# Kernel optimization log

Measured on AMD Instinct MI355X. Metric: run time of the kernel, lower is better.

Reference implementation:

```python
import jax, jax.numpy as jnp
import numpy as np

D_MODEL = 1024
D_FF = 4096
N_EXPERTS = 8
D_EXPERT = D_FF // N_EXPERTS  # 512
TOP_K = 2
LB_WEIGHT = 0.01
B, S = 4, 2048


def setup_inputs() -> dict:
    key = jax.random.key(0)
    ks = jax.random.split(key, 8)
    x = jax.random.normal(ks[0], (B, S, D_MODEL), dtype=jnp.float32)
    # per-expert FFN params stacked on expert axis
    w1 = jax.random.normal(ks[1], (N_EXPERTS, D_MODEL, D_EXPERT), dtype=jnp.float32) * (1.0 / np.sqrt(D_MODEL))
    b1 = jnp.zeros((N_EXPERTS, D_EXPERT), dtype=jnp.float32)
    w2 = jax.random.normal(ks[2], (N_EXPERTS, D_EXPERT, D_MODEL), dtype=jnp.float32) * (1.0 / np.sqrt(D_EXPERT))
    b2 = jnp.zeros((N_EXPERTS, D_MODEL), dtype=jnp.float32)
    centroids = jax.random.normal(ks[3], (N_EXPERTS, D_MODEL), dtype=jnp.float32) * 0.02
    w_route = jax.random.normal(ks[4], (N_EXPERTS, D_MODEL), dtype=jnp.float32) * (1.0 / np.sqrt(D_MODEL))
    return {"x": x, "w1": w1, "b1": b1, "w2": w2, "b2": b2,
            "centroids": centroids, "w_route": w_route}


def _top_k_softmax(logits, k):
    # softmax restricted to the top-k logits per token; zeros elsewhere
    vals, _ = jax.lax.top_k(logits, k)          # (..., k)
    thresh = vals[..., -1:]                     # kth-largest value
    masked = jnp.where(logits >= thresh, logits, -jnp.inf)
    return jax.nn.softmax(masked, axis=-1)


def reference(x, w1, b1, w2, b2, centroids, w_route):
    eps = 1e-12
    x_norm = x / jnp.maximum(jnp.linalg.norm(x, axis=-1, keepdims=True), eps)
    c_norm = centroids / jnp.maximum(jnp.linalg.norm(centroids, axis=-1, keepdims=True), eps)
    cos_scores = jnp.einsum('bsd,ed->bse', x_norm, c_norm)
    route_scores = jnp.einsum('bsd,ed->bse', x, w_route)
    logits = cos_scores + route_scores                       # (B,S,E)
    gates = _top_k_softmax(logits, TOP_K)                    # (B,S,E)
    # all experts computed on all tokens (dense MoE, masked combine)
    h = jax.nn.gelu(jnp.einsum('bsd,edh->bseh', x, w1) + b1, approximate=False)
    expert_out = jnp.einsum('bseh,ehd->bsed', h, w2) + b2    # (B,S,E,D)
    out = jnp.einsum('bse,bsed->bsd', gates, expert_out)
    return out
```

## Files before the change

kernel.cpp:

```cpp
#include <hip/hip_runtime.h>
#include <hip/hip_bf16.h>
#include <math.h>

#define T_TOK 8192
#define DM 1024
#define DE 512
#define NE 8
#define DFF 4096

#define CO_X   0
#define CO_W1  8388608
#define CO_W2  12582912
#define CO_B1  16777216
#define CO_B2  16781312
#define CO_CE  16789504
#define CO_WR  16797696
#define CO_TOT 16805888

#define WS_GATE2 256
#define WS_B32   65792
#define WS_TOP2  262400
#define WS_TOK   295168
#define WS_AE    360704
#define WS_AG    426240
#define WS_INV   491776
#define WS_CONV  557312
#define WS_HC    34169088
#define WS_OC    50946304

typedef __attribute__((ext_vector_type(8))) __bf16 bf16x8;
typedef __attribute__((ext_vector_type(4))) __bf16 bf16x4;
typedef __attribute__((ext_vector_type(4))) float f32x4;

__device__ __forceinline__ f32x4 ld4(const void* p, size_t off, int md)
{
  f32x4 r;
  if (md){
    bf16x4 v = *(const bf16x4*)((const __bf16*)p + off);
    #pragma unroll
    for (int j = 0; j < 4; j++) r[j] = (float)v[j];
  } else {
    r = *(const f32x4*)((const float*)p + off);
  }
  return r;
}

__device__ __forceinline__ void async_ld16(const __bf16* g, __bf16* l)
{
  __builtin_amdgcn_global_load_lds(
      (const __attribute__((address_space(1))) unsigned int*)g,
      (__attribute__((address_space(3))) unsigned int*)l, 16, 0, 0);
}

__global__ __launch_bounds__(256) void detect_k(const void* xp, const void* cp,
                                                int* meta, int* b32)
{
  const int tid = threadIdx.x;
  const float* xf = (const float*)xp;
  int ok = 0;
  for (int i = tid; i < 1024; i += 256){
    float a = fabsf(xf[i]);
    if (a > 1e-8f && a < 100.f) ok++;
  }
  __shared__ int cnt;
  __shared__ int flg;
  if (tid == 0) cnt = 0;
  __syncthreads();
  atomicAdd(&cnt, ok);
  __syncthreads();
  if (tid == 0){ flg = (cnt > 512) ? 0 : 1; meta[0] = flg; }
  __syncthreads();
  const int md = flg;

  const int e = tid >> 5, i = tid & 31;
  float ss = 0.f;
  for (int j = 0; j < 32; j++){
    size_t d = (size_t)e * DM + i + j * 32;
    float v = md ? (float)((const __bf16*)cp)[d] : ((const float*)cp)[d];
    ss += v * v;
  }
  #pragma unroll
  for (int m = 1; m < 32; m <<= 1) ss += __shfl_xor(ss, m, 64);
  float* cinv = (float*)(meta + 48);
  if (i == 0) cinv[e] = 1.f / fmaxf(sqrtf(ss), 1e-12f);

  b32[tid] = 0;
  if (tid < 8) meta[16 + tid] = 0;
}

__global__ __launch_bounds__(256) void convert_k(
    const float* __restrict__ b1, const float* __restrict__ b2,
    const float* __restrict__ ce, const float* __restrict__ wr,
    __bf16* __restrict__ dst, const int* __restrict__ meta)
{
  if (meta[0]) return;
  const size_t j = ((size_t)blockIdx.x * 256 + threadIdx.x) * 4;
  const float* src;
  const size_t doff = CO_B1 + j;
  if      (j < 4096)  src = b1 + j;
  else if (j < 12288) src = b2 + (j - 4096);
  else if (j < 20480) src = ce + (j - 12288);
  else                src = wr + (j - 20480);
  f32x4 v = *(const f32x4*)src;
  bf16x4 o;
  #pragma unroll
  for (int t = 0; t < 4; t++) o[t] = (__bf16)v[t];
  *(bf16x4*)(dst + doff) = o;
}

__global__ __launch_bounds__(256) void transp_k(
    const void* w1q, const void* w2q, __bf16* __restrict__ conv,
    const int* __restrict__ meta)
{
  const int md = meta[0];
  __shared__ __bf16 tile[32][33];
  const int b = blockIdx.x, tid = threadIdx.x;
  const int ty = tid >> 5, tx = tid & 31;

  const void* src; __bf16* dst; int ldS, ldD, i0, j0; size_t soff, doffb;
  if (b < 4096){
    const int e = b >> 9, t = b & 511;
    i0 = (t >> 4) << 5; j0 = (t & 15) << 5;
    ldS = DE; ldD = DM;
    soff = (size_t)e * DM * DE;
    dst = conv + CO_W1; doffb = (size_t)e * DE * DM;
    src = md ? (const void*)((const __bf16*)w1q) : (const void*)((const float*)w1q);
  } else {
    const int e = (b - 4096) >> 9, t = (b - 4096) & 511;
    i0 = (t >> 5) << 5; j0 = (t & 31) << 5;
    ldS = DM; ldD = DE;
    soff = (size_t)e * DE * DM;
    dst = conv + CO_W2; doffb = (size_t)e * DM * DE;
    src = md ? (const void*)((const __bf16*)w2q) : (const void*)((const float*)w2q);
  }

  #pragma unroll
  for (int rr = 0; rr < 4; rr++){
    const int r = rr * 8 + ty;
    const size_t s = soff + (size_t)(i0 + r) * ldS + j0 + tx;
    tile[r][tx] = md ? ((const __bf16*)src)[s] : (__bf16)((const float*)src)[s];
  }
  __syncthreads();
  #pragma unroll
  for (int rr = 0; rr < 4; rr++){
    const int r = rr * 8 + ty;
    dst[doffb + (size_t)(j0 + r) * ldD + i0 + tx] = tile[tx][r];
  }
}

__global__ __launch_bounds__(256) void route_k(
    const void* __restrict__ xp, const void* __restrict__ cp,
    const void* __restrict__ wp, const int* __restrict__ meta,
    __bf16* __restrict__ conv, float2* __restrict__ gate2,
    int* __restrict__ top2, int* __restrict__ b32)
{
  const int md = meta[0];
  const float* cinv = (const float*)(meta + 48);
  const int tid = threadIdx.x;
  const int g = tid >> 4, l = tid & 15;
  const int t = blockIdx.x * 16 + g;

  __shared__ int hist[8];
  if (tid < 8) hist[tid] = 0;
  __syncthreads();

  float xx = 0.f, cd[NE], wd[NE];
  #pragma unroll
  for (int e = 0; e < NE; e++){ cd[e] = 0.f; wd[e] = 0.f; }

  const size_t xbase = (size_t)t * DM;
  for (int j = 0; j < 16; j++){
    const int d0 = j * 64 + l * 4;
    f32x4 xv = ld4(xp, xbase + d0, md);
    if (!md){
      bf16x4 o;
      #pragma unroll
      for (int jj = 0; jj < 4; jj++) o[jj] = (__bf16)xv[jj];
      *(bf16x4*)(conv + CO_X + xbase + d0) = o;
    }
    xx += xv[0]*xv[0] + xv[1]*xv[1] + xv[2]*xv[2] + xv[3]*xv[3];
    #pragma unroll
    for (int e = 0; e < NE; e++){
      f32x4 cv = ld4(cp, (size_t)e * DM + d0, md);
      f32x4 wv = ld4(wp, (size_t)e * DM + d0, md);
      cd[e] += xv[0]*cv[0] + xv[1]*cv[1] + xv[2]*cv[2] + xv[3]*cv[3];
      wd[e] += xv[0]*wv[0] + xv[1]*wv[1] + xv[2]*wv[2] + xv[3]*wv[3];
    }
  }
  #pragma unroll
  for (int m = 1; m < 16; m <<= 1){
    xx += __shfl_xor(xx, m, 64);
    #pragma unroll
    for (int e = 0; e < NE; e++){
      cd[e] += __shfl_xor(cd[e], m, 64);
      wd[e] += __shfl_xor(wd[e], m, 64);
    }
  }

  if (l == 0){
    const float rxn = 1.f / fmaxf(sqrtf(xx), 1e-12f);
    float logits[NE];
    #pragma unroll
    for (int e = 0; e < NE; e++) logits[e] = cd[e] * rxn * cinv[e] + wd[e];
    float m1 = -1e30f; int i1 = 0;
    #pragma unroll
    for (int e = 0; e < NE; e++) if (logits[e] > m1){ m1 = logits[e]; i1 = e; }
    float m2 = -1e30f; int i2 = (i1 == 0) ? 1 : 0;
    #pragma unroll
    for (int e = 0; e < NE; e++)
      if (e != i1 && logits[e] > m2){ m2 = logits[e]; i2 = e; }
    float denom = 0.f, ex1 = 0.f, ex2 = 0.f;
    #pragma unroll
    for (int e = 0; e < NE; e++){
      if (logits[e] >= m2){
        float ee = expf(logits[e] - m1);
        denom += ee;
        if (e == i1) ex1 = ee;
        if (e == i2) ex2 = ee;
      }
    }
    const float inv = 1.f / denom;
    gate2[t] = make_float2(ex1 * inv, ex2 * inv);
    top2[t] = i1 | (i2 << 8);
    atomicAdd(&hist[i1], 1);
    atomicAdd(&hist[i2], 1);
  }
  __syncthreads();
  if (tid < 8) atomicAdd(&b32[(blockIdx.x >> 4) * 8 + tid], hist[tid]);
}

__global__ void offsets_k(int* meta, int* b32)
{
  const int l = threadIdx.x;
  int running = 0;
  for (int e = 0; e < NE; e++){
    int v = (l < 32) ? b32[l * 8 + e] : 0;
    int incl = v;
    #pragma unroll
    for (int ofs = 1; ofs < 32; ofs <<= 1){
      int n = __shfl_up(incl, ofs, 64);
      if (l >= ofs) incl += n;
    }
    int tot = __shfl(incl, 31, 64);
    if (l < 32) b32[l * 8 + e] = running + (incl - v);
    if (l == 0){ meta[16 + e] = tot; meta[32 + e] = running; }
    running += tot;
  }
}

__global__ __launch_bounds__(256) void place_k(
    const int* __restrict__ top2, const float2* __restrict__ gate2,
    const int* __restrict__ b32, int* __restrict__ tok, int* __restrict__ ae,
    float* __restrict__ agv, int* __restrict__ inv)
{
  __shared__ int cur[8];
  if (threadIdx.x < 8) cur[threadIdx.x] = b32[blockIdx.x * 8 + threadIdx.x];
  __syncthreads();
  const int t = blockIdx.x * 256 + threadIdx.x;
  const int p = top2[t];
  const float2 gg = gate2[t];
  const int e1 = p & 255, e2 = (p >> 8) & 255;
  const int s1 = atomicAdd(&cur[e1], 1);
  tok[s1] = t; ae[s1] = e1; agv[s1] = gg.x; inv[2 * t] = s1;
  const int s2 = atomicAdd(&cur[e2], 1);
  tok[s2] = t; ae[s2] = e2; agv[s2] = gg.y; inv[2 * t + 1] = s2;
}

__device__ __forceinline__ bool find_tile(const int* meta, int tm,
                                          int& e, int& base, int& valid)
{
  for (e = 0; e < NE; e++){
    const int cnt = meta[16 + e];
    const int nt = (cnt + 127) >> 7;
    if (tm < nt){
      const int r0 = tm << 7;
      base = meta[32 + e] + r0;
      valid = cnt - r0;
      return true;
    }
    tm -= nt;
  }
  return false;
}

__device__ __forceinline__ bool find_tile256(const int* meta, int tm,
                                             int& e, int& base, int& valid)
{
  for (e = 0; e < NE; e++){
    const int cnt = meta[16 + e];
    const int nt = (cnt + 255) >> 8;
    if (tm < nt){
      const int r0 = tm << 8;
      base = meta[32 + e] + r0;
      valid = cnt - r0;
      return true;
    }
    tm -= nt;
  }
  return false;
}

__global__ __launch_bounds__(512, 2) void gemm1g_k(
    const void* xq, const void* b1q, const __bf16* __restrict__ conv,
    const int* __restrict__ meta, const int* __restrict__ tok,
    const float* __restrict__ agv, __bf16* __restrict__ Hc)
{
  const int md = meta[0];
  const __bf16* X  = md ? (const __bf16*)xq : conv + CO_X;
  const __bf16* WT = conv + CO_W1;
  const __bf16* bb = md ? (const __bf16*)b1q : conv + CO_B1;

  int e, base, valid;
  if (!find_tile(meta, blockIdx.x, e, base, valid)) return;
  const int n0 = blockIdx.y * 128;

  __shared__ __attribute__((aligned(16))) __bf16 As[2][128 * 64];
  __shared__ __attribute__((aligned(16))) __bf16 Bs[2][128 * 64];

  const int tid = threadIdx.x;
  const int wv = tid >> 6, lane = tid & 63;
  const int q = lane >> 4, ln = lane & 15;
  const int wm = (wv >> 2) * 64, wn = (wv & 3) * 32;
  const int swz = ln & 7;
  f32x4 acc[4][2] = {};

  const int srow = tid >> 3, sch = tid & 7;
  const int sx = ((sch ^ (srow & 7)) << 3);
  const int ta = tok[base + ((srow      < valid) ? srow      : 0)];
  const int tb = tok[base + ((srow + 64 < valid) ? srow + 64 : 0)];
  const __bf16* Ag0 = X + (size_t)ta * DM + sx;
  const __bf16* Ag1 = X + (size_t)tb * DM + sx;
  const __bf16* Bg0 = WT + (size_t)e * (DE * DM) + (size_t)(n0 + srow) * DM + sx;
  const __bf16* Bg1 = Bg0 + (size_t)64 * DM;

  #define G1_STAGE(BUF, K0)                                   \
    do {                                                      \
      async_ld16(Ag0 + (K0), &As[BUF][tid * 8]);              \
      async_ld16(Ag1 + (K0), &As[BUF][tid * 8 + 4096]);       \
      async_ld16(Bg0 + (K0), &Bs[BUF][tid * 8]);              \
      async_ld16(Bg1 + (K0), &Bs[BUF][tid * 8 + 4096]);       \
    } while (0)

  #define G1_COMPUTE(BUF)                                                      \
    do {                                                                       \
      _Pragma("unroll")                                                        \
      for (int kk = 0; kk < 2; kk++){                                          \
        bf16x8 af[4], bfr[2];                                                  \
        const int ch = (((kk << 2) | q) ^ swz) << 3;                           \
        _Pragma("unroll")                                                      \
        for (int mi = 0; mi < 4; mi++)                                         \
          af[mi] = *(const bf16x8*)&As[BUF][(wm + mi * 16 + ln) * 64 + ch];    \
        _Pragma("unroll")                                                      \
        for (int ni = 0; ni < 2; ni++)                                         \
          bfr[ni] = *(const bf16x8*)&Bs[BUF][(wn + ni * 16 + ln) * 64 + ch];   \
        _Pragma("unroll")                                                      \
        for (int mi = 0; mi < 4; mi++)                                         \
          _Pragma("unroll")                                                    \
          for (int ni = 0; ni < 2; ni++)                                       \
            acc[mi][ni] = __builtin_amdgcn_mfma_f32_16x16x32_bf16(             \
                af[mi], bfr[ni], acc[mi][ni], 0, 0, 0);                        \
      }                                                                        \
    } while (0)

  G1_STAGE(0, 0);
  __syncthreads();
  int cr = 0;
  for (int t = 0; t < 16; ++t){
    if (t < 15) G1_STAGE(cr ^ 1, (t + 1) * 64);
    G1_COMPUTE(cr);
    __syncthreads();
    cr ^= 1;
  }
  #undef G1_STAGE
  #undef G1_COMPUTE

  const int coln = n0 + wn;
  float bset[2];
  #pragma unroll
  for (int ni = 0; ni < 2; ni++)
    bset[ni] = (float)bb[e * DE + coln + ni * 16 + ln];
  #pragma unroll
  for (int mi = 0; mi < 4; mi++){
    #pragma unroll
    for (int r = 0; r < 4; r++){
      const int row = wm + mi * 16 + q * 4 + r;
      if (row < valid){
        const int slot = base + row;
        const float g = agv[slot];
        #pragma unroll
        for (int ni = 0; ni < 2; ni++){
          float v = acc[mi][ni][r] + bset[ni];
          float h = 0.5f * v * (1.0f + erff(v * 0.70710678118654752f));
          Hc[(size_t)slot * DE + coln + ni * 16 + ln] = (__bf16)(g * h);
        }
      }
    }
  }
}

__global__ __launch_bounds__(512, 2) void gemm2g_k(
    const __bf16* __restrict__ Hc, const __bf16* __restrict__ conv,
    const int* __restrict__ meta, __bf16* __restrict__ Oc)
{
  const __bf16* WT = conv + CO_W2;

  int e, base, valid;
  if (!find_tile256(meta, blockIdx.x, e, base, valid)) return;
  const int n0 = blockIdx.y * 256;

  __shared__ __attribute__((aligned(16))) __bf16 As[2][256 * 64];
  __shared__ __attribute__((aligned(16))) __bf16 Bs[2][256 * 64];

  const int tid = threadIdx.x;
  const int wv = tid >> 6, lane = tid & 63;
  const int q = lane >> 4, ln = lane & 15;
  const int wm = (wv >> 2) * 128, wn = (wv & 3) * 64;
  const int swz = ln & 7;
  f32x4 acc[8][4] = {};

  const int srow = tid >> 3, sch = tid & 7;
  const int sx = ((sch ^ (srow & 7)) << 3);
  const int r0 = (srow       < valid) ? srow       : 0;
  const int r1 = (srow +  64 < valid) ? srow +  64 : 0;
  const int r2 = (srow + 128 < valid) ? srow + 128 : 0;
  const int r3 = (srow + 192 < valid) ? srow + 192 : 0;
  const __bf16* Ag0 = Hc + (size_t)(base + r0) * DE + sx;
  const __bf16* Ag1 = Hc + (size_t)(base + r1) * DE + sx;
  const __bf16* Ag2 = Hc + (size_t)(base + r2) * DE + sx;
  const __bf16* Ag3 = Hc + (size_t)(base + r3) * DE + sx;
  const __bf16* Bg0 = WT + (size_t)e * (DM * DE) + (size_t)(n0 + srow) * DE + sx;

  #define G2_STAGE(BUF, K0)                                          \
    do {                                                             \
      async_ld16(Ag0 + (K0), &As[BUF][tid * 8]);                     \
      async_ld16(Ag1 + (K0), &As[BUF][tid * 8 + 4096]);              \
      async_ld16(Ag2 + (K0), &As[BUF][tid * 8 + 8192]);              \
      async_ld16(Ag3 + (K0), &As[BUF][tid * 8 + 12288]);             \
      async_ld16(Bg0 + (K0),                &Bs[BUF][tid * 8]);      \
      async_ld16(Bg0 + (K0) +  64 * DE,     &Bs[BUF][tid * 8 + 4096]);  \
      async_ld16(Bg0 + (K0) + 128 * DE,     &Bs[BUF][tid * 8 + 8192]);  \
      async_ld16(Bg0 + (K0) + 192 * DE,     &Bs[BUF][tid * 8 + 12288]); \
    } while (0)

  #define G2_COMPUTE(BUF)                                                      \
    do {                                                                       \
      _Pragma("unroll")                                                        \
      for (int kk = 0; kk < 2; kk++){                                          \
        bf16x8 af[8], bfr[4];                                                  \
        const int ch = (((kk << 2) | q) ^ swz) << 3;                           \
        _Pragma("unroll")                                                      \
        for (int mi = 0; mi < 8; mi++)                                         \
          af[mi] = *(const bf16x8*)&As[BUF][(wm + mi * 16 + ln) * 64 + ch];    \
        _Pragma("unroll")                                                      \
        for (int ni = 0; ni < 4; ni++)                                         \
          bfr[ni] = *(const bf16x8*)&Bs[BUF][(wn + ni * 16 + ln) * 64 + ch];   \
        _Pragma("unroll")                                                      \
        for (int mi = 0; mi < 8; mi++)                                         \
          _Pragma("unroll")                                                    \
          for (int ni = 0; ni < 4; ni++)                                       \
            acc[mi][ni] = __builtin_amdgcn_mfma_f32_16x16x32_bf16(             \
                af[mi], bfr[ni], acc[mi][ni], 0, 0, 0);                        \
      }                                                                        \
    } while (0)

  G2_STAGE(0, 0);
  __syncthreads();
  int cr = 0;
  for (int t = 0; t < 8; ++t){
    if (t < 7) G2_STAGE(cr ^ 1, (t + 1) * 64);
    G2_COMPUTE(cr);
    __syncthreads();
    cr ^= 1;
  }
  #undef G2_STAGE
  #undef G2_COMPUTE

  #pragma unroll
  for (int mi = 0; mi < 8; mi++){
    #pragma unroll
    for (int r = 0; r < 4; r++){
      const int row = wm + mi * 16 + q * 4 + r;
      if (row < valid){
        const int slot = base + row;
        #pragma unroll
        for (int ni = 0; ni < 4; ni++)
          Oc[(size_t)slot * DM + n0 + wn + ni * 16 + ln] = (__bf16)acc[mi][ni][r];
      }
    }
  }
}

__global__ __launch_bounds__(256) void combine_k(
    const __bf16* __restrict__ Oc, const int* __restrict__ inv,
    const int* __restrict__ ae, const float* __restrict__ agv,
    const void* b2q, const int* __restrict__ meta, void* out)
{
  const int md = meta[0];
  const int t = blockIdx.x;
  const int s1 = inv[2 * t], s2 = inv[2 * t + 1];
  const int e1 = ae[s1], e2 = ae[s2];
  const float g1 = agv[s1], g2 = agv[s2];
  const int c = threadIdx.x * 4;

  bf16x4 o1 = *(const bf16x4*)(Oc + (size_t)s1 * DM + c);
  bf16x4 o2 = *(const bf16x4*)(Oc + (size_t)s2 * DM + c);
  f32x4 bv1 = ld4(b2q, (size_t)e1 * DM + c, md);
  f32x4 bv2 = ld4(b2q, (size_t)e2 * DM + c, md);
  f32x4 rr;
  #pragma unroll
  for (int j = 0; j < 4; j++)
    rr[j] = (float)o1[j] + (float)o2[j] + g1 * bv1[j] + g2 * bv2[j];

  if (md){
    bf16x4 ob;
    #pragma unroll
    for (int j = 0; j < 4; j++) ob[j] = (__bf16)rr[j];
    *(bf16x4*)((__bf16*)out + (size_t)t * DM + c) = ob;
  } else {
    *(f32x4*)((float*)out + (size_t)t * DM + c) = rr;
  }
}

extern "C" void kernel_launch(void* const* d_in, const int* in_sizes, int n_in,
                              void* d_out, int out_size, void* d_ws, size_t ws_size,
                              hipStream_t stream)
{
  char* ws = (char*)d_ws;
  int*    meta  = (int*)ws;
  float2* gate2 = (float2*)(ws + WS_GATE2);
  int*    b32   = (int*)(ws + WS_B32);
  int*    top2  = (int*)(ws + WS_TOP2);
  int*    tok   = (int*)(ws + WS_TOK);
  int*    ae    = (int*)(ws + WS_AE);
  float*  agv   = (float*)(ws + WS_AG);
  int*    inv   = (int*)(ws + WS_INV);
  __bf16* conv  = (__bf16*)(ws + WS_CONV);
  __bf16* Hc    = (__bf16*)(ws + WS_HC);
  __bf16* Oc    = (__bf16*)(ws + WS_OC);

  detect_k<<<1, 256, 0, stream>>>(d_in[0], d_in[5], meta, b32);
  transp_k<<<8192, 256, 0, stream>>>(d_in[1], d_in[3], conv, meta);
  convert_k<<<28, 256, 0, stream>>>(
      (const float*)d_in[2], (const float*)d_in[4], (const float*)d_in[5],
      (const float*)d_in[6], conv, meta);
  route_k<<<T_TOK / 16, 256, 0, stream>>>(d_in[0], d_in[5], d_in[6], meta,
                                          conv, gate2, top2, b32);
  offsets_k<<<1, 64, 0, stream>>>(meta, b32);
  place_k<<<T_TOK / 256, 256, 0, stream>>>(top2, gate2, b32, tok, ae, agv, inv);
  gemm1g_k<<<dim3(136, 4), 512, 0, stream>>>(d_in[0], d_in[2], conv, meta,
                                             tok, agv, Hc);
  gemm2g_k<<<dim3(72, 4), 512, 0, stream>>>(Hc, conv, meta, Oc);
  combine_k<<<T_TOK, 256, 0, stream>>>(Oc, inv, ae, agv, d_in[4], meta, d_out);
}
```

Before: 250.5 us.

## Use 256x256 tiles in first grouped GEMM, interleave expert tile mapping, drop LDS swizzle

The first expert GEMM now uses 256x256 output tiles with 8x4 MFMA accumulators per wave, matching the second GEMM, and launches a 256x2 grid. Both GEMMs map blocks to experts directly (expert = blockIdx.x & 7) instead of scanning expert counts, which spreads experts across blocks but launches many blocks that exit early. The XOR swizzle on shared-memory chunk columns is removed in both GEMMs, which may bring back LDS bank conflicts. Larger tiles raise data reuse but cut the number of useful blocks and occupancy, and use more registers.

```diff
diff --git a/kernel.cpp b/kernel.cpp
--- a/kernel.cpp
+++ b/kernel.cpp
@@ -266,38 +266,16 @@
   tok[s2] = t; ae[s2] = e2; agv[s2] = gg.y; inv[2 * t + 1] = s2;
 }
 
-__device__ __forceinline__ bool find_tile(const int* meta, int tm,
-                                          int& e, int& base, int& valid)
-{
-  for (e = 0; e < NE; e++){
-    const int cnt = meta[16 + e];
-    const int nt = (cnt + 127) >> 7;
-    if (tm < nt){
-      const int r0 = tm << 7;
-      base = meta[32 + e] + r0;
-      valid = cnt - r0;
-      return true;
-    }
-    tm -= nt;
-  }
-  return false;
-}
-
-__device__ __forceinline__ bool find_tile256(const int* meta, int tm,
+__device__ __forceinline__ bool find_slot256(const int* meta, int bx,
                                              int& e, int& base, int& valid)
 {
-  for (e = 0; e < NE; e++){
-    const int cnt = meta[16 + e];
-    const int nt = (cnt + 255) >> 8;
-    if (tm < nt){
-      const int r0 = tm << 8;
-      base = meta[32 + e] + r0;
-      valid = cnt - r0;
-      return true;
-    }
-    tm -= nt;
-  }
-  return false;
+  e = bx & 7;
+  const int cnt = meta[16 + e];
+  const int r0 = (bx >> 3) << 8;
+  if (r0 >= cnt) return false;
+  base = meta[32 + e] + r0;
+  valid = cnt - r0;
+  return true;
 }
 
 __global__ __launch_bounds__(512, 2) void gemm1g_k(
@@ -311,143 +289,47 @@
   const __bf16* bb = md ? (const __bf16*)b1q : conv + CO_B1;
 
   int e, base, valid;
-  if (!find_tile(meta, blockIdx.x, e, base, valid)) return;
-  const int n0 = blockIdx.y * 128;
-
-  __shared__ __attribute__((aligned(16))) __bf16 As[2][128 * 64];
-  __shared__ __attribute__((aligned(16))) __bf16 Bs[2][128 * 64];
+  if (!find_slot256(meta, blockIdx.x, e, base, valid)) return;
+  const int n0 = blockIdx.y * 256;
+
+  __shared__ __attribute__((aligned(16))) __bf16 As[2][256 * 64];
+  __shared__ __attribute__((aligned(16))) __bf16 Bs[2][256 * 64];
 
   const int tid = threadIdx.x;
   const int wv = tid >> 6, lane = tid & 63;
   const int q = lane >> 4, ln = lane & 15;
-  const int wm = (wv >> 2) * 64, wn = (wv & 3) * 32;
-  const int swz = ln & 7;
-  f32x4 acc[4][2] = {};
-
-  const int srow = tid >> 3, sch = tid & 7;
-  const int sx = ((sch ^ (srow & 7)) << 3);
-  const int ta = tok[base + ((srow      < valid) ? srow      : 0)];
-  const int tb = tok[base + ((srow + 64 < valid) ? srow + 64 : 0)];
-  const __bf16* Ag0 = X + (size_t)ta * DM + sx;
-  const __bf16* Ag1 = X + (size_t)tb * DM + sx;
-  const __bf16* Bg0 = WT + (size_t)e * (DE * DM) + (size_t)(n0 + srow) * DM + sx;
-  const __bf16* Bg1 = Bg0 + (size_t)64 * DM;
-
-  #define G1_STAGE(BUF, K0)                                   \
-    do {                                                      \
-      async_ld16(Ag0 + (K0), &As[BUF][tid * 8]);              \
-      async_ld16(Ag1 + (K0), &As[BUF][tid * 8 + 4096]);       \
-      async_ld16(Bg0 + (K0), &Bs[BUF][tid * 8]);              \
-      async_ld16(Bg1 + (K0), &Bs[BUF][tid * 8 + 4096]);       \
+  const int wm = (wv >> 2) * 128, wn = (wv & 3) * 64;
+  f32x4 acc[8][4] = {};
+
+  const int srow = tid >> 3, sc = (tid & 7) * 8;
+  const int t0 = tok[base + ((srow       < valid) ? srow       : 0)];
+  const int t1 = tok[base + ((srow +  64 < valid) ? srow +  64 : 0)];
+  const int t2 = tok[base + ((srow + 128 < valid) ? srow + 128 : 0)];
+  const int t3 = tok[base + ((srow + 192 < valid) ? srow + 192 : 0)];
+  const __bf16* Ag0 = X + (size_t)t0 * DM + sc;
+  const __bf16* Ag1 = X + (size_t)t1 * DM + sc;
+  const __bf16* Ag2 = X + (size_t)t2 * DM + sc;
+  const __bf16* Ag3 = X + (size_t)t3 * DM + sc;
+  const __bf16* Bg  = WT + (size_t)e * (DE * DM) + (size_t)(n0 + srow) * DM + sc;
+
+  #define G1_STAGE(BUF, K0)                                        \
+    do {                                                           \
+      async_ld16(Ag0 + (K0), &As[BUF][tid * 8]);                   \
+      async_ld16(Ag1 + (K0), &As[BUF][tid * 8 + 4096]);            \
+      async_ld16(Ag2 + (K0), &As[BUF][tid * 8 + 8192]);            \
+      async_ld16(Ag3 + (K0), &As[BUF][tid * 8 + 12288]);           \
+      async_ld16(Bg  + (K0),             &Bs[BUF][tid * 8]);       \
+      async_ld16(Bg  + (K0) +  64 * DM,  &Bs[BUF][tid * 8 + 4096]);  \
+      async_ld16(Bg  + (K0) + 128 * DM,  &Bs[BUF][tid * 8 + 8192]);  \
+      async_ld16(Bg  + (K0) + 192 * DM,  &Bs[BUF][tid * 8 + 12288]); \
     } while (0)
 
   #define G1_COMPUTE(BUF)                                                      \
     do {                                                                       \
       _Pragma("unroll")                                                        \
       for (int kk = 0; kk < 2; kk++){                                          \
-        bf16x8 af[4], bfr[2];                                                  \
-        const int ch = (((kk << 2) | q) ^ swz) << 3;                           \
-        _Pragma("unroll")                                                      \
-        for (int mi = 0; mi < 4; mi++)                                         \
-          af[mi] = *(const bf16x8*)&As[BUF][(wm + mi * 16 + ln) * 64 + ch];    \
-        _Pragma("unroll")                                                      \
-        for (int ni = 0; ni < 2; ni++)                                         \
-          bfr[ni] = *(const bf16x8*)&Bs[BUF][(wn + ni * 16 + ln) * 64 + ch];   \
-        _Pragma("unroll")                                                      \
-        for (int mi = 0; mi < 4; mi++)                                         \
-          _Pragma("unroll")                                                    \
-          for (int ni = 0; ni < 2; ni++)                                       \
-            acc[mi][ni] = __builtin_amdgcn_mfma_f32_16x16x32_bf16(             \
-                af[mi], bfr[ni], acc[mi][ni], 0, 0, 0);                        \
-      }                                                                        \
-    } while (0)
-
-  G1_STAGE(0, 0);
-  __syncthreads();
-  int cr = 0;
-  for (int t = 0; t < 16; ++t){
-    if (t < 15) G1_STAGE(cr ^ 1, (t + 1) * 64);
-    G1_COMPUTE(cr);
-    __syncthreads();
-    cr ^= 1;
-  }
-  #undef G1_STAGE
-  #undef G1_COMPUTE
-
-  const int coln = n0 + wn;
-  float bset[2];
-  #pragma unroll
-  for (int ni = 0; ni < 2; ni++)
-    bset[ni] = (float)bb[e * DE + coln + ni * 16 + ln];
-  #pragma unroll
-  for (int mi = 0; mi < 4; mi++){
-    #pragma unroll
-    for (int r = 0; r < 4; r++){
-      const int row = wm + mi * 16 + q * 4 + r;
-      if (row < valid){
-        const int slot = base + row;
-        const float g = agv[slot];
-        #pragma unroll
-        for (int ni = 0; ni < 2; ni++){
-          float v = acc[mi][ni][r] + bset[ni];
-          float h = 0.5f * v * (1.0f + erff(v * 0.70710678118654752f));
-          Hc[(size_t)slot * DE + coln + ni * 16 + ln] = (__bf16)(g * h);
-        }
-      }
-    }
-  }
-}
-
-__global__ __launch_bounds__(512, 2) void gemm2g_k(
-    const __bf16* __restrict__ Hc, const __bf16* __restrict__ conv,
-    const int* __restrict__ meta, __bf16* __restrict__ Oc)
-{
-  const __bf16* WT = conv + CO_W2;
-
-  int e, base, valid;
-  if (!find_tile256(meta, blockIdx.x, e, base, valid)) return;
-  const int n0 = blockIdx.y * 256;
-
-  __shared__ __attribute__((aligned(16))) __bf16 As[2][256 * 64];
-  __shared__ __attribute__((aligned(16))) __bf16 Bs[2][256 * 64];
-
-  const int tid = threadIdx.x;
-  const int wv = tid >> 6, lane = tid & 63;
-  const int q = lane >> 4, ln = lane & 15;
-  const int wm = (wv >> 2) * 128, wn = (wv & 3) * 64;
-  const int swz = ln & 7;
-  f32x4 acc[8][4] = {};
-
-  const int srow = tid >> 3, sch = tid & 7;
-  const int sx = ((sch ^ (srow & 7)) << 3);
-  const int r0 = (srow       < valid) ? srow       : 0;
-  const int r1 = (srow +  64 < valid) ? srow +  64 : 0;
-  const int r2 = (srow + 128 < valid) ? srow + 128 : 0;
-  const int r3 = (srow + 192 < valid) ? srow + 192 : 0;
-  const __bf16* Ag0 = Hc + (size_t)(base + r0) * DE + sx;
-  const __bf16* Ag1 = Hc + (size_t)(base + r1) * DE + sx;
-  const __bf16* Ag2 = Hc + (size_t)(base + r2) * DE + sx;
-  const __bf16* Ag3 = Hc + (size_t)(base + r3) * DE + sx;
-  const __bf16* Bg0 = WT + (size_t)e * (DM * DE) + (size_t)(n0 + srow) * DE + sx;
-
-  #define G2_STAGE(BUF, K0)                                          \
-    do {                                                             \
-      async_ld16(Ag0 + (K0), &As[BUF][tid * 8]);                     \
-      async_ld16(Ag1 + (K0), &As[BUF][tid * 8 + 4096]);              \
-      async_ld16(Ag2 + (K0), &As[BUF][tid * 8 + 8192]);              \
-      async_ld16(Ag3 + (K0), &As[BUF][tid * 8 + 12288]);             \
-      async_ld16(Bg0 + (K0),                &Bs[BUF][tid * 8]);      \
-      async_ld16(Bg0 + (K0) +  64 * DE,     &Bs[BUF][tid * 8 + 4096]);  \
-      async_ld16(Bg0 + (K0) + 128 * DE,     &Bs[BUF][tid * 8 + 8192]);  \
-      async_ld16(Bg0 + (K0) + 192 * DE,     &Bs[BUF][tid * 8 + 12288]); \
-    } while (0)
-
-  #define G2_COMPUTE(BUF)                                                      \
-    do {                                                                       \
-      _Pragma("unroll")                                                        \
-      for (int kk = 0; kk < 2; kk++){                                          \
         bf16x8 af[8], bfr[4];                                                  \
-        const int ch = (((kk << 2) | q) ^ swz) << 3;                           \
+        const int ch = (kk * 4 + q) * 8;                                       \
         _Pragma("unroll")                                                      \
         for (int mi = 0; mi < 8; mi++)                                         \
           af[mi] = *(const bf16x8*)&As[BUF][(wm + mi * 16 + ln) * 64 + ch];    \
@@ -463,6 +345,105 @@
       }                                                                        \
     } while (0)
 
+  G1_STAGE(0, 0);
+  __syncthreads();
+  int cr = 0;
+  for (int t = 0; t < 16; ++t){
+    if (t < 15) G1_STAGE(cr ^ 1, (t + 1) * 64);
+    G1_COMPUTE(cr);
+    __syncthreads();
+    cr ^= 1;
+  }
+  #undef G1_STAGE
+  #undef G1_COMPUTE
+
+  const int coln = n0 + wn;
+  float bset[4];
+  #pragma unroll
+  for (int ni = 0; ni < 4; ni++)
+    bset[ni] = (float)bb[e * DE + coln + ni * 16 + ln];
+  #pragma unroll
+  for (int mi = 0; mi < 8; mi++){
+    #pragma unroll
+    for (int r = 0; r < 4; r++){
+      const int row = wm + mi * 16 + q * 4 + r;
+      if (row < valid){
+        const int slot = base + row;
+        const float g = agv[slot];
+        #pragma unroll
+        for (int ni = 0; ni < 4; ni++){
+          float v = acc[mi][ni][r] + bset[ni];
+          float h = 0.5f * v * (1.0f + erff(v * 0.70710678118654752f));
+          Hc[(size_t)slot * DE + coln + ni * 16 + ln] = (__bf16)(g * h);
+        }
+      }
+    }
+  }
+}
+
+__global__ __launch_bounds__(512, 2) void gemm2g_k(
+    const __bf16* __restrict__ Hc, const __bf16* __restrict__ conv,
+    const int* __restrict__ meta, __bf16* __restrict__ Oc)
+{
+  const __bf16* WT = conv + CO_W2;
+
+  int e, base, valid;
+  if (!find_slot256(meta, blockIdx.x, e, base, valid)) return;
+  const int n0 = blockIdx.y * 256;
+
+  __shared__ __attribute__((aligned(16))) __bf16 As[2][256 * 64];
+  __shared__ __attribute__((aligned(16))) __bf16 Bs[2][256 * 64];
+
+  const int tid = threadIdx.x;
+  const int wv = tid >> 6, lane = tid & 63;
+  const int q = lane >> 4, ln = lane & 15;
+  const int wm = (wv >> 2) * 128, wn = (wv & 3) * 64;
+  f32x4 acc[8][4] = {};
+
+  const int srow = tid >> 3, sc = (tid & 7) * 8;
+  const int r0 = (srow       < valid) ? srow       : 0;
+  const int r1 = (srow +  64 < valid) ? srow +  64 : 0;
+  const int r2 = (srow + 128 < valid) ? srow + 128 : 0;
+  const int r3 = (srow + 192 < valid) ? srow + 192 : 0;
+  const __bf16* Ag0 = Hc + (size_t)(base + r0) * DE + sc;
+  const __bf16* Ag1 = Hc + (size_t)(base + r1) * DE + sc;
+  const __bf16* Ag2 = Hc + (size_t)(base + r2) * DE + sc;
+  const __bf16* Ag3 = Hc + (size_t)(base + r3) * DE + sc;
+  const __bf16* Bg  = WT + (size_t)e * (DM * DE) + (size_t)(n0 + srow) * DE + sc;
+
+  #define G2_STAGE(BUF, K0)                                        \
+    do {                                                           \
+      async_ld16(Ag0 + (K0), &As[BUF][tid * 8]);                   \
+      async_ld16(Ag1 + (K0), &As[BUF][tid * 8 + 4096]);            \
+      async_ld16(Ag2 + (K0), &As[BUF][tid * 8 + 8192]);            \
+      async_ld16(Ag3 + (K0), &As[BUF][tid * 8 + 12288]);           \
+      async_ld16(Bg  + (K0),             &Bs[BUF][tid * 8]);       \
+      async_ld16(Bg  + (K0) +  64 * DE,  &Bs[BUF][tid * 8 + 4096]);  \
+      async_ld16(Bg  + (K0) + 128 * DE,  &Bs[BUF][tid * 8 + 8192]);  \
+      async_ld16(Bg  + (K0) + 192 * DE,  &Bs[BUF][tid * 8 + 12288]); \
+    } while (0)
+
+  #define G2_COMPUTE(BUF)                                                      \
+    do {                                                                       \
+      _Pragma("unroll")                                                        \
+      for (int kk = 0; kk < 2; kk++){                                          \
+        bf16x8 af[8], bfr[4];                                                  \
+        const int ch = (kk * 4 + q) * 8;                                       \
+        _Pragma("unroll")                                                      \
+        for (int mi = 0; mi < 8; mi++)                                         \
+          af[mi] = *(const bf16x8*)&As[BUF][(wm + mi * 16 + ln) * 64 + ch];    \
+        _Pragma("unroll")                                                      \
+        for (int ni = 0; ni < 4; ni++)                                         \
+          bfr[ni] = *(const bf16x8*)&Bs[BUF][(wn + ni * 16 + ln) * 64 + ch];   \
+        _Pragma("unroll")                                                      \
+        for (int mi = 0; mi < 8; mi++)                                         \
+          _Pragma("unroll")                                                    \
+          for (int ni = 0; ni < 4; ni++)                                       \
+            acc[mi][ni] = __builtin_amdgcn_mfma_f32_16x16x32_bf16(             \
+                af[mi], bfr[ni], acc[mi][ni], 0, 0, 0);                        \
+      }                                                                        \
+    } while (0)
+
   G2_STAGE(0, 0);
   __syncthreads();
   int cr = 0;
@@ -547,8 +528,8 @@
                                           conv, gate2, top2, b32);
   offsets_k<<<1, 64, 0, stream>>>(meta, b32);
   place_k<<<T_TOK / 256, 256, 0, stream>>>(top2, gate2, b32, tok, ae, agv, inv);
-  gemm1g_k<<<dim3(136, 4), 512, 0, stream>>>(d_in[0], d_in[2], conv, meta,
+  gemm1g_k<<<dim3(256, 2), 512, 0, stream>>>(d_in[0], d_in[2], conv, meta,
                                              tok, agv, Hc);
-  gemm2g_k<<<dim3(72, 4), 512, 0, stream>>>(Hc, conv, meta, Oc);
+  gemm2g_k<<<dim3(256, 4), 512, 0, stream>>>(Hc, conv, meta, Oc);
   combine_k<<<T_TOK, 256, 0, stream>>>(Oc, inv, ae, agv, d_in[4], meta, d_out);
 }
```

Result: slower. 275.5 us (+10.0%).
